# Performance work log

Hardware: AMD Instinct MI355X
Metric: run time of the kernel (lower is better)

## Reference

```python
import jax, jax.numpy as jnp
import numpy as np

N_NODES = 100000
N_EDGES = 3200000
F_IN, H_ENC, H_GCN, H_Q, A_DIM = 128, 128, 128, 256, 10


def setup_inputs() -> dict:
    key = jax.random.key(0)
    ks = jax.random.split(key, 8)
    s = lambda d: 1.0 / np.sqrt(d)
    return {
        "x": jax.random.normal(ks[0], (N_NODES, F_IN), jnp.float32),
        "edge_index": jax.random.randint(ks[1], (2, N_EDGES), 0, N_NODES, jnp.int64),
        "W_enc": jax.random.normal(ks[2], (F_IN, H_ENC), jnp.float32) * s(F_IN),
        "b_enc": jnp.zeros((H_ENC,), jnp.float32),
        "W_gcn": jax.random.normal(ks[3], (H_ENC, H_GCN), jnp.float32) * s(H_ENC),
        "b_gcn": jnp.zeros((H_GCN,), jnp.float32),
        "W1": jax.random.normal(ks[4], (H_GCN, H_Q), jnp.float32) * s(H_GCN),
        "b1": jnp.zeros((H_Q,), jnp.float32),
        "W2": jax.random.normal(ks[5], (H_Q, A_DIM), jnp.float32) * s(H_Q),
        "b2": jnp.zeros((A_DIM,), jnp.float32),
    }


def gcn_conv(x, edge_index, W, b):
    # Standard GCNConv: D^{-1/2} (A + I) D^{-1/2} X W + b, symmetric norm with self-loops.
    n = x.shape[0]
    src, dst = edge_index[0], edge_index[1]
    xw = x @ W  # [N, H]
    deg = jnp.ones((n,), xw.dtype).at[dst].add(1.0)  # in-degree + self-loop
    dinv = jax.lax.rsqrt(deg)
    coef = dinv[src] * dinv[dst]  # [E]
    msg = xw[src] * coef[:, None]  # [E, H] gather-scale
    agg = jax.ops.segment_sum(msg, dst, num_segments=n)  # scatter-add
    agg = agg + xw * (dinv * dinv)[:, None]  # self-loop contribution
    return agg + b


def reference(x, edge_index, W_enc, b_enc, W_gcn, b_gcn, W1, b1, W2, b2):
    h = jax.nn.relu(x @ W_enc + b_enc)              # Encoder: Linear + ReLU
    h = jax.nn.relu(gcn_conv(h, edge_index, W_gcn, b_gcn))  # GCNConv + ReLU
    q = jax.nn.relu(h @ W1 + b1) @ W2 + b2          # Q_Net MLP
    return q
```

## Files before the change

### kernel.cpp

```cpp
#include <hip/hip_runtime.h>

#define N_NODES 100000
constexpr int F     = 128;
constexpr int NB    = (N_NODES + 63) / 64;
constexpr int BCAP  = 2560;
constexpr int LCAP  = 80;
constexpr int CHUNK = 8192;
constexpr int PADN  = N_NODES;

typedef __attribute__((ext_vector_type(8))) short short8;
typedef __attribute__((ext_vector_type(4))) float f32x4;
typedef __attribute__((ext_vector_type(4))) short short4v;

__device__ inline short f2bf(float v) {
    union { float f; unsigned u; } x; x.f = v;
    unsigned r = (x.u + 0x7fff + ((x.u >> 16) & 1)) >> 16;
    return (short)r;
}
__device__ inline float lo_bf(unsigned v) {
    union { unsigned u; float f; } x; x.u = v << 16; return x.f;
}
__device__ inline float hi_bf(unsigned v) {
    union { unsigned u; float f; } x; x.u = v & 0xffff0000u; return x.f;
}

__global__ __launch_bounds__(256) void prep_kernel(const float* __restrict__ W_enc,
                                                   const float* __restrict__ W_gcn,
                                                   const float* __restrict__ W1,
                                                   const float* __restrict__ W2,
                                                   short* __restrict__ Wte,
                                                   short* __restrict__ Wtg,
                                                   short* __restrict__ Wt1,
                                                   short* __restrict__ W2t,
                                                   int* __restrict__ bcr) {
    int idx = blockIdx.x * 256 + threadIdx.x;
    if (idx < 16384) { int h = idx >> 7, k = idx & 127; Wte[idx] = f2bf(W_enc[k * 128 + h]); return; }
    idx -= 16384;
    if (idx < 16384) { int h = idx >> 7, k = idx & 127; Wtg[idx] = f2bf(W_gcn[k * 128 + h]); return; }
    idx -= 16384;
    if (idx < 32768) { int h = idx >> 7, k = idx & 127; Wt1[idx] = f2bf(W1[k * 256 + h]); return; }
    idx -= 32768;
    if (idx < 4096)  { int n = idx >> 8, k = idx & 255; W2t[idx] = (n < 10) ? f2bf(W2[k * 10 + n]) : (short)0; return; }
    idx -= 4096;
    if (idx < NB) bcr[idx] = 0;
}

__global__ __launch_bounds__(512) void part_kernel(const int* __restrict__ src,
                                                   const int* __restrict__ dst,
                                                   int* __restrict__ bcur,
                                                   int* __restrict__ part, int E) {
    __shared__ int cnt[NB];
    __shared__ int base[NB];
    for (int b = threadIdx.x; b < NB; b += 512) cnt[b] = 0;
    __syncthreads();
    const int e0 = blockIdx.x * CHUNK;
    const int e1 = min(e0 + CHUNK, E);
#pragma unroll 4
    for (int e = e0 + threadIdx.x; e < e1; e += 512)
        atomicAdd(&cnt[dst[e] >> 6], 1);
    __syncthreads();
    for (int b = threadIdx.x; b < NB; b += 512) {
        int c = cnt[b];
        base[b] = c ? atomicAdd(&bcur[b], c) : 0;
        cnt[b] = 0;
    }
    __syncthreads();
#pragma unroll 4
    for (int e = e0 + threadIdx.x; e < e1; e += 512) {
        int d = dst[e];
        int b = d >> 6;
        int idx = base[b] + atomicAdd(&cnt[b], 1);
        if (idx < BCAP) part[b * BCAP + idx] = src[e] | ((d & 63) << 17);
    }
}

__global__ __launch_bounds__(256) void gemmA_kernel(const float* __restrict__ x,
                                                    const short* __restrict__ Wte,
                                                    const short* __restrict__ Wtg,
                                                    const float* __restrict__ b_enc,
                                                    const int* __restrict__ bcur,
                                                    const int* __restrict__ part,
                                                    short* __restrict__ xs) {
    __shared__ int deg_l[64];
    __shared__ short h_l[4][16][136];
    const int b = blockIdx.x;
    if (threadIdx.x < 64) deg_l[threadIdx.x] = 0;
    __syncthreads();
    const int cnt = min(bcur[b], BCAP);
    const int* p = part + (size_t)b * BCAP;
#pragma unroll 4
    for (int i = threadIdx.x; i < cnt; i += 256)
        atomicAdd(&deg_l[(p[i] >> 17) & 63], 1);

    const int wave = threadIdx.x >> 6;
    const int lane = threadIdx.x & 63;
    const int quad = lane >> 4;
    const int l16  = lane & 15;
    const int node0 = b * 64 + wave * 16;
    int nrow = node0 + l16;
    const bool valid = nrow < N_NODES;
    if (!valid) nrow = N_NODES - 1;

    f32x4 acc[8] = {};
#pragma unroll
    for (int kc = 0; kc < 4; ++kc) {
        const float* ap = x + (size_t)nrow * 128 + kc * 32 + quad * 8;
        float4 f0 = *reinterpret_cast<const float4*>(ap);
        float4 f1 = *reinterpret_cast<const float4*>(ap + 4);
        short8 xfrag;
        xfrag.s0 = f2bf(f0.x); xfrag.s1 = f2bf(f0.y); xfrag.s2 = f2bf(f0.z); xfrag.s3 = f2bf(f0.w);
        xfrag.s4 = f2bf(f1.x); xfrag.s5 = f2bf(f1.y); xfrag.s6 = f2bf(f1.z); xfrag.s7 = f2bf(f1.w);
#pragma unroll
        for (int t = 0; t < 8; ++t) {
            short8 wfrag = *reinterpret_cast<const short8*>(Wte + (size_t)(t * 16 + l16) * 128 + kc * 32 + quad * 8);
            acc[t] = __builtin_amdgcn_mfma_f32_16x16x32_bf16(wfrag, xfrag, acc[t], 0, 0, 0);
        }
    }
#pragma unroll
    for (int t = 0; t < 8; ++t) {
        short4v o;
#pragma unroll
        for (int r = 0; r < 4; ++r)
            ((short*)&o)[r] = f2bf(fmaxf(acc[t][r] + b_enc[t * 16 + quad * 4 + r], 0.f));
        *reinterpret_cast<short4v*>(&h_l[wave][l16][t * 16 + quad * 4]) = o;
    }
    __syncthreads();

    const float dvn = rsqrtf(1.f + (float)deg_l[wave * 16 + l16]);
    f32x4 acc2[8] = {};
#pragma unroll
    for (int kc = 0; kc < 4; ++kc) {
        short8 xfrag = *reinterpret_cast<const short8*>(&h_l[wave][l16][kc * 32 + quad * 8]);
#pragma unroll
        for (int t = 0; t < 8; ++t) {
            short8 wfrag = *reinterpret_cast<const short8*>(Wtg + (size_t)(t * 16 + l16) * 128 + kc * 32 + quad * 8);
            acc2[t] = __builtin_amdgcn_mfma_f32_16x16x32_bf16(wfrag, xfrag, acc2[t], 0, 0, 0);
        }
    }
    const int srow = node0 + l16;
#pragma unroll
    for (int t = 0; t < 8; ++t) {
        short4v o;
#pragma unroll
        for (int r = 0; r < 4; ++r)
            ((short*)&o)[r] = valid ? f2bf(acc2[t][r] * dvn) : (short)0;
        *reinterpret_cast<short4v*>(xs + (size_t)srow * 128 + t * 16 + quad * 4) = o;
    }
}

__global__ __launch_bounds__(256) void agg_kernel(const short* __restrict__ xs,
                                                  const int* __restrict__ bcur,
                                                  const int* __restrict__ part,
                                                  const float* __restrict__ bg,
                                                  short* __restrict__ h2) {
    __shared__ int csr_l[64 * LCAP];
    __shared__ int cur[64];
    const int b = blockIdx.x;
    const int tid = threadIdx.x;
    if (tid < 64) cur[tid] = 0;
    __syncthreads();
    const int cnt = min(bcur[b], BCAP);
    const int* p = part + (size_t)b * BCAP;
#pragma unroll 4
    for (int i = tid; i < cnt; i += 256) {
        int v = p[i];
        int ld = (v >> 17) & 63;
        int pos = atomicAdd(&cur[ld], 1);
        if (pos < LCAP) csr_l[ld * LCAP + pos] = v & 0x1FFFF;
    }
    __syncthreads();
    if (tid < 64) {
        int d = min(cur[tid], LCAP);
        int dp = (d + 7) & ~7;
        for (int k = d; k < dp; ++k) csr_l[tid * LCAP + k] = PADN;
    }
    __syncthreads();

    const int wave = tid >> 6;
    const int lane = tid & 63;
    const int half = lane >> 5;
    const int fl   = lane & 31;
    const uint2* xs2 = reinterpret_cast<const uint2*>(xs);
    const float4 bg4 = reinterpret_cast<const float4*>(bg)[fl];

    for (int t = 0; t < 16; ++t) {
        const int ld = wave * 16 + t;
        const int node = b * 64 + ld;
        if (node >= N_NODES) break;

        const int dtrue = cur[ld];
        const int dpad = (min(dtrue, LCAP) + 7) & ~7;
        const float dv = rsqrtf(1.f + (float)dtrue);
        const int* cl = csr_l + ld * LCAP;

        float a0 = 0.f, a1 = 0.f, a2 = 0.f, a3 = 0.f;
        for (int j = 0; j < dpad; j += 8) {
#pragma unroll
            for (int u = 0; u < 4; ++u) {
                int sj = cl[j + u * 2 + half];
                uint2 v = xs2[((size_t)sj << 5) + fl];
                a0 += lo_bf(v.x); a1 += hi_bf(v.x);
                a2 += lo_bf(v.y); a3 += hi_bf(v.y);
            }
        }
        a0 += __shfl_xor(a0, 32, 64);
        a1 += __shfl_xor(a1, 32, 64);
        a2 += __shfl_xor(a2, 32, 64);
        a3 += __shfl_xor(a3, 32, 64);
        uint2 vs = xs2[((size_t)node << 5) + fl];
        a0 += lo_bf(vs.x); a1 += hi_bf(vs.x);
        a2 += lo_bf(vs.y); a3 += hi_bf(vs.y);
        a0 = fmaxf(fmaf(a0, dv, bg4.x), 0.f);
        a1 = fmaxf(fmaf(a1, dv, bg4.y), 0.f);
        a2 = fmaxf(fmaf(a2, dv, bg4.z), 0.f);
        a3 = fmaxf(fmaf(a3, dv, bg4.w), 0.f);
        if (lane < 32) {
            uint2 o;
            o.x = (unsigned)(unsigned short)f2bf(a0) | ((unsigned)(unsigned short)f2bf(a1) << 16);
            o.y = (unsigned)(unsigned short)f2bf(a2) | ((unsigned)(unsigned short)f2bf(a3) << 16);
            reinterpret_cast<uint2*>(h2)[((size_t)node << 5) + fl] = o;
        }
    }
}

__global__ __launch_bounds__(256) void gemmB_kernel(const short* __restrict__ h2,
                                                    const short* __restrict__ Wt1,
                                                    const short* __restrict__ W2t,
                                                    const float* __restrict__ b1,
                                                    const float* __restrict__ b2,
                                                    float* __restrict__ q) {
    __shared__ short hq_l[4][16][264];
    const int wave = threadIdx.x >> 6;
    const int lane = threadIdx.x & 63;
    const int quad = lane >> 4;
    const int l16  = lane & 15;
    const int node0 = blockIdx.x * 64 + wave * 16;
    int nrow = node0 + l16;
    if (nrow >= N_NODES) nrow = N_NODES - 1;

    f32x4 acc[16] = {};
#pragma unroll
    for (int kc = 0; kc < 4; ++kc) {
        short8 xfrag = *reinterpret_cast<const short8*>(h2 + (size_t)nrow * 128 + kc * 32 + quad * 8);
#pragma unroll
        for (int t = 0; t < 16; ++t) {
            short8 wfrag = *reinterpret_cast<const short8*>(Wt1 + (size_t)(t * 16 + l16) * 128 + kc * 32 + quad * 8);
            acc[t] = __builtin_amdgcn_mfma_f32_16x16x32_bf16(wfrag, xfrag, acc[t], 0, 0, 0);
        }
    }
#pragma unroll
    for (int t = 0; t < 16; ++t) {
        short4v o;
#pragma unroll
        for (int r = 0; r < 4; ++r)
            ((short*)&o)[r] = f2bf(fmaxf(acc[t][r] + b1[t * 16 + quad * 4 + r], 0.f));
        *reinterpret_cast<short4v*>(&hq_l[wave][l16][t * 16 + quad * 4]) = o;
    }

    f32x4 a2 = {};
#pragma unroll
    for (int kc = 0; kc < 8; ++kc) {
        short8 afrag = *reinterpret_cast<const short8*>(&hq_l[wave][l16][kc * 32 + quad * 8]);
        short8 bfrag = *reinterpret_cast<const short8*>(W2t + (size_t)l16 * 256 + kc * 32 + quad * 8);
        a2 = __builtin_amdgcn_mfma_f32_16x16x32_bf16(afrag, bfrag, a2, 0, 0, 0);
    }
    if (l16 < 10) {
        float bv = b2[l16];
#pragma unroll
        for (int r = 0; r < 4; ++r) {
            int nd = node0 + quad * 4 + r;
            if (nd < N_NODES) q[(size_t)nd * 10 + l16] = a2[r] + bv;
        }
    }
}

extern "C" void kernel_launch(void* const* d_in, const int* in_sizes, int n_in,
                              void* d_out, int out_size, void* d_ws, size_t ws_size,
                              hipStream_t stream) {
    const float* x     = (const float*)d_in[0];
    const int*   ei    = (const int*)d_in[1];
    const float* W_enc = (const float*)d_in[2];
    const float* b_enc = (const float*)d_in[3];
    const float* W_gcn = (const float*)d_in[4];
    const float* b_gcn = (const float*)d_in[5];
    const float* W1    = (const float*)d_in[6];
    const float* b1    = (const float*)d_in[7];
    const float* W2    = (const float*)d_in[8];
    const float* b2    = (const float*)d_in[9];
    float* q = (float*)d_out;

    const int E = in_sizes[1] / 2;
    const int* srcv = ei;
    const int* dstv = ei + E;

    char* ws = (char*)d_ws;
    const size_t XSB = (size_t)(NB * 64) * 128 * sizeof(short);
    short* xs  = (short*)(ws);
    short* h2  = (short*)(ws + XSB);
    int*   part= (int*)  (ws + 2 * XSB);
    char*  tail = ws + 2 * XSB + (size_t)NB * BCAP * sizeof(int);
    int*   bcr = (int*)(tail);
    short* Wte = (short*)(tail + 8192);
    short* Wtg = (short*)(tail + 8192 + 32768);
    short* Wt1 = (short*)(tail + 8192 + 65536);
    short* W2t = (short*)(tail + 8192 + 131072);

    prep_kernel<<<279, 256, 0, stream>>>(W_enc, W_gcn, W1, W2, Wte, Wtg, Wt1, W2t, bcr);
    part_kernel<<<(E + CHUNK - 1) / CHUNK, 512, 0, stream>>>(srcv, dstv, bcr, part, E);
    gemmA_kernel<<<NB, 256, 0, stream>>>(x, Wte, Wtg, b_enc, bcr, part, xs);
    agg_kernel<<<NB, 256, 0, stream>>>(xs, bcr, part, b_gcn, h2);
    gemmB_kernel<<<NB, 256, 0, stream>>>(h2, Wt1, W2t, b1, b2, q);
}
```

Measured before the change: 407.8 us.

## Fuse GCN aggregation with Q-net MLP and widen gather loads to 16B

```diff
diff --git a/kernel.cpp b/kernel.cpp
--- a/kernel.cpp
+++ b/kernel.cpp
@@ -11,6 +11,7 @@
 typedef __attribute__((ext_vector_type(8))) short short8;
 typedef __attribute__((ext_vector_type(4))) float f32x4;
 typedef __attribute__((ext_vector_type(4))) short short4v;
+typedef __attribute__((ext_vector_type(4))) unsigned uint4v;
 
 __device__ inline short f2bf(float v) {
     union { float f; unsigned u; } x; x.f = v;
@@ -148,13 +149,20 @@
     }
 }
 
-__global__ __launch_bounds__(256) void agg_kernel(const short* __restrict__ xs,
-                                                  const int* __restrict__ bcur,
-                                                  const int* __restrict__ part,
-                                                  const float* __restrict__ bg,
-                                                  short* __restrict__ h2) {
-    __shared__ int csr_l[64 * LCAP];
-    __shared__ int cur[64];
+__global__ __launch_bounds__(256, 3) void aggB_kernel(const short* __restrict__ xs,
+                                                      const int* __restrict__ bcur,
+                                                      const int* __restrict__ part,
+                                                      const float* __restrict__ bg,
+                                                      const short* __restrict__ Wt1,
+                                                      const short* __restrict__ W2t,
+                                                      const float* __restrict__ b1,
+                                                      const float* __restrict__ b2,
+                                                      float* __restrict__ q) {
+    __shared__ char smemA[64 * LCAP * 4 > 4 * 16 * 264 * 2 ? 64 * LCAP * 4 : 4 * 16 * 264 * 2 + 256];
+    __shared__ short h2_l[4][16][136];
+    int* csr_l = (int*)smemA;
+    int* cur   = (int*)(smemA + 64 * LCAP * 4);
+
     const int b = blockIdx.x;
     const int tid = threadIdx.x;
     if (tid < 64) cur[tid] = 0;
@@ -178,10 +186,11 @@
 
     const int wave = tid >> 6;
     const int lane = tid & 63;
-    const int half = lane >> 5;
-    const int fl   = lane & 31;
-    const uint2* xs2 = reinterpret_cast<const uint2*>(xs);
-    const float4 bg4 = reinterpret_cast<const float4*>(bg)[fl];
+    const int g    = lane >> 4;
+    const int l16  = lane & 15;
+    const uint4v* xs4 = reinterpret_cast<const uint4v*>(xs);
+    const float4 bgA = reinterpret_cast<const float4*>(bg)[l16 * 2];
+    const float4 bgB = reinterpret_cast<const float4*>(bg)[l16 * 2 + 1];
 
     for (int t = 0; t < 16; ++t) {
         const int ld = wave * 16 + t;
@@ -193,55 +202,54 @@
         const float dv = rsqrtf(1.f + (float)dtrue);
         const int* cl = csr_l + ld * LCAP;
 
-        float a0 = 0.f, a1 = 0.f, a2 = 0.f, a3 = 0.f;
+        float a0 = 0.f, a1 = 0.f, a2 = 0.f, a3 = 0.f, a4 = 0.f, a5 = 0.f, a6 = 0.f, a7 = 0.f;
         for (int j = 0; j < dpad; j += 8) {
 #pragma unroll
-            for (int u = 0; u < 4; ++u) {
-                int sj = cl[j + u * 2 + half];
-                uint2 v = xs2[((size_t)sj << 5) + fl];
+            for (int u = 0; u < 2; ++u) {
+                int sj = cl[j + u * 4 + g];
+                uint4v v = xs4[((size_t)sj << 4) + l16];
                 a0 += lo_bf(v.x); a1 += hi_bf(v.x);
                 a2 += lo_bf(v.y); a3 += hi_bf(v.y);
+                a4 += lo_bf(v.z); a5 += hi_bf(v.z);
+                a6 += lo_bf(v.w); a7 += hi_bf(v.w);
             }
         }
-        a0 += __shfl_xor(a0, 32, 64);
-        a1 += __shfl_xor(a1, 32, 64);
-        a2 += __shfl_xor(a2, 32, 64);
-        a3 += __shfl_xor(a3, 32, 64);
-        uint2 vs = xs2[((size_t)node << 5) + fl];
-        a0 += lo_bf(vs.x); a1 += hi_bf(vs.x);
-        a2 += lo_bf(vs.y); a3 += hi_bf(vs.y);
-        a0 = fmaxf(fmaf(a0, dv, bg4.x), 0.f);
-        a1 = fmaxf(fmaf(a1, dv, bg4.y), 0.f);
-        a2 = fmaxf(fmaf(a2, dv, bg4.z), 0.f);
-        a3 = fmaxf(fmaf(a3, dv, bg4.w), 0.f);
-        if (lane < 32) {
-            uint2 o;
-            o.x = (unsigned)(unsigned short)f2bf(a0) | ((unsigned)(unsigned short)f2bf(a1) << 16);
-            o.y = (unsigned)(unsigned short)f2bf(a2) | ((unsigned)(unsigned short)f2bf(a3) << 16);
-            reinterpret_cast<uint2*>(h2)[((size_t)node << 5) + fl] = o;
-        }
-    }
-}
-
-__global__ __launch_bounds__(256) void gemmB_kernel(const short* __restrict__ h2,
-                                                    const short* __restrict__ Wt1,
-                                                    const short* __restrict__ W2t,
-                                                    const float* __restrict__ b1,
-                                                    const float* __restrict__ b2,
-                                                    float* __restrict__ q) {
-    __shared__ short hq_l[4][16][264];
-    const int wave = threadIdx.x >> 6;
-    const int lane = threadIdx.x & 63;
+        a0 += __shfl_xor(a0, 16, 64); a0 += __shfl_xor(a0, 32, 64);
+        a1 += __shfl_xor(a1, 16, 64); a1 += __shfl_xor(a1, 32, 64);
+        a2 += __shfl_xor(a2, 16, 64); a2 += __shfl_xor(a2, 32, 64);
+        a3 += __shfl_xor(a3, 16, 64); a3 += __shfl_xor(a3, 32, 64);
+        a4 += __shfl_xor(a4, 16, 64); a4 += __shfl_xor(a4, 32, 64);
+        a5 += __shfl_xor(a5, 16, 64); a5 += __shfl_xor(a5, 32, 64);
+        a6 += __shfl_xor(a6, 16, 64); a6 += __shfl_xor(a6, 32, 64);
+        a7 += __shfl_xor(a7, 16, 64); a7 += __shfl_xor(a7, 32, 64);
+        if (g == 0) {
+            uint4v vs = xs4[((size_t)node << 4) + l16];
+            a0 += lo_bf(vs.x); a1 += hi_bf(vs.x);
+            a2 += lo_bf(vs.y); a3 += hi_bf(vs.y);
+            a4 += lo_bf(vs.z); a5 += hi_bf(vs.z);
+            a6 += lo_bf(vs.w); a7 += hi_bf(vs.w);
+            short8 o;
+            o.s0 = f2bf(fmaxf(fmaf(a0, dv, bgA.x), 0.f));
+            o.s1 = f2bf(fmaxf(fmaf(a1, dv, bgA.y), 0.f));
+            o.s2 = f2bf(fmaxf(fmaf(a2, dv, bgA.z), 0.f));
+            o.s3 = f2bf(fmaxf(fmaf(a3, dv, bgA.w), 0.f));
+            o.s4 = f2bf(fmaxf(fmaf(a4, dv, bgB.x), 0.f));
+            o.s5 = f2bf(fmaxf(fmaf(a5, dv, bgB.y), 0.f));
+            o.s6 = f2bf(fmaxf(fmaf(a6, dv, bgB.z), 0.f));
+            o.s7 = f2bf(fmaxf(fmaf(a7, dv, bgB.w), 0.f));
+            *reinterpret_cast<short8*>(&h2_l[wave][ld - wave * 16][l16 * 8]) = o;
+        }
+    }
+    __syncthreads();
+    short* hq_l = (short*)smemA;
+
     const int quad = lane >> 4;
-    const int l16  = lane & 15;
-    const int node0 = blockIdx.x * 64 + wave * 16;
-    int nrow = node0 + l16;
-    if (nrow >= N_NODES) nrow = N_NODES - 1;
+    const int node0 = b * 64 + wave * 16;
 
     f32x4 acc[16] = {};
 #pragma unroll
     for (int kc = 0; kc < 4; ++kc) {
-        short8 xfrag = *reinterpret_cast<const short8*>(h2 + (size_t)nrow * 128 + kc * 32 + quad * 8);
+        short8 xfrag = *reinterpret_cast<const short8*>(&h2_l[wave][l16][kc * 32 + quad * 8]);
 #pragma unroll
         for (int t = 0; t < 16; ++t) {
             short8 wfrag = *reinterpret_cast<const short8*>(Wt1 + (size_t)(t * 16 + l16) * 128 + kc * 32 + quad * 8);
@@ -254,13 +262,13 @@
 #pragma unroll
         for (int r = 0; r < 4; ++r)
             ((short*)&o)[r] = f2bf(fmaxf(acc[t][r] + b1[t * 16 + quad * 4 + r], 0.f));
-        *reinterpret_cast<short4v*>(&hq_l[wave][l16][t * 16 + quad * 4]) = o;
+        *reinterpret_cast<short4v*>(&hq_l[(wave * 16 + l16) * 264 + t * 16 + quad * 4]) = o;
     }
 
     f32x4 a2 = {};
 #pragma unroll
     for (int kc = 0; kc < 8; ++kc) {
-        short8 afrag = *reinterpret_cast<const short8*>(&hq_l[wave][l16][kc * 32 + quad * 8]);
+        short8 afrag = *reinterpret_cast<const short8*>(&hq_l[(wave * 16 + l16) * 264 + kc * 32 + quad * 8]);
         short8 bfrag = *reinterpret_cast<const short8*>(W2t + (size_t)l16 * 256 + kc * 32 + quad * 8);
         a2 = __builtin_amdgcn_mfma_f32_16x16x32_bf16(afrag, bfrag, a2, 0, 0, 0);
     }
@@ -296,9 +304,8 @@
     char* ws = (char*)d_ws;
     const size_t XSB = (size_t)(NB * 64) * 128 * sizeof(short);
     short* xs  = (short*)(ws);
-    short* h2  = (short*)(ws + XSB);
-    int*   part= (int*)  (ws + 2 * XSB);
-    char*  tail = ws + 2 * XSB + (size_t)NB * BCAP * sizeof(int);
+    int*   part= (int*)  (ws + XSB);
+    char*  tail = ws + XSB + (size_t)NB * BCAP * sizeof(int);
     int*   bcr = (int*)(tail);
     short* Wte = (short*)(tail + 8192);
     short* Wtg = (short*)(tail + 8192 + 32768);
@@ -308,6 +315,5 @@
     prep_kernel<<<279, 256, 0, stream>>>(W_enc, W_gcn, W1, W2, Wte, Wtg, Wt1, W2t, bcr);
     part_kernel<<<(E + CHUNK - 1) / CHUNK, 512, 0, stream>>>(srcv, dstv, bcr, part, E);
     gemmA_kernel<<<NB, 256, 0, stream>>>(x, Wte, Wtg, b_enc, bcr, part, xs);
-    agg_kernel<<<NB, 256, 0, stream>>>(xs, bcr, part, b_gcn, h2);
-    gemmB_kernel<<<NB, 256, 0, stream>>>(h2, Wt1, W2t, b1, b2, q);
-}
+    aggB_kernel<<<NB, 256, 0, stream>>>(xs, bcr, part, b_gcn, Wt1, W2t, b1, b2, q);
+}
```

Measured after the change: 402.3 us. No clear change (-1.4%).
